# Kernel tuning notes

Measured on AMD Instinct MI355X. Metric: run time of the kernel, lower is better.

## Reference

```python
import jax, jax.numpy as jnp
import numpy as np
import math

PC_MIN_X, PC_MIN_Y = 0.0, -40.0
VOXEL = 0.05
STRIDE = 8
PE_CH = 16
NEG_SLOPE = 0.01
BN_EPS = 1e-5


def _grid_points():
    # get_pseudo_points: centers of stride-8 BEV cells
    xs = np.arange(0.2, 70.4, 0.4, dtype=np.float32)    # 176
    ys = np.arange(-39.8, 40.2, 0.4, dtype=np.float32)  # 200
    gx, gy = np.meshgrid(xs, ys)                        # (200, 176)
    return jnp.asarray(np.stack([gx, gy], -1).reshape(-1, 2))  # [P, 2]


def _pe3d(D, H, W):
    ch = PE_CH
    div = jnp.exp(jnp.arange(0, ch, 2, dtype=jnp.float32) * (-math.log(10000.0) / ch))
    def enc(n):
        t = jnp.arange(n, dtype=jnp.float32)[:, None] * div[None, :]
        return jnp.concatenate([jnp.sin(t), jnp.cos(t)], axis=-1)  # [n, ch]
    pex = jnp.broadcast_to(enc(D)[:, None, None, :], (D, H, W, ch))
    pey = jnp.broadcast_to(enc(H)[None, :, None, :], (D, H, W, ch))
    pez = jnp.broadcast_to(enc(W)[None, None, :, :], (D, H, W, ch))
    return jnp.concatenate([pex, pey, pez], axis=-1).transpose(3, 0, 1, 2)  # [3*ch, D, H, W]


def _bn_lrelu(h, g, b):
    # eval-mode BatchNorm3d with running_mean=0, running_var=1, then LeakyReLU(0.01)
    h = h * (g / np.sqrt(1.0 + BN_EPS))[None, :, None, None, None] + b[None, :, None, None, None]
    return jnp.where(h >= 0, h, NEG_SLOPE * h)


def _dvf(x, w1, b1, g1, be1, w2, b2, g2, be2, w3, b3):
    N, C, D, H, W = x.shape
    pe = _pe3d(D, H, W)  # [48, D, H, W]
    feats = jnp.concatenate([x, jnp.broadcast_to(pe[None], (N,) + pe.shape)], axis=1)
    h = jnp.einsum('ncdhw,oc->nodhw', feats, w1) + b1[None, :, None, None, None]
    h = _bn_lrelu(h, g1, be1)
    h = jnp.einsum('ncdhw,oc->nodhw', h, w2) + b2[None, :, None, None, None]
    h = _bn_lrelu(h, g2, be2)
    logits = jnp.einsum('ncdhw,oc->nodhw', h, w3) + b3[None, :, None, None, None]  # [N,1,D,H,W]
    wts = jax.nn.softmax(logits, axis=2)  # softmax over depth D
    return (x * wts).reshape(N, C * D, H, W)


def _bilinear(im, x, y):
    # im: (H, W, C), x/y: (P,)  -- faithful to bilinear_interpolate_torch
    H, W = im.shape[0], im.shape[1]
    xf = jnp.floor(x).astype(jnp.int32)
    yf = jnp.floor(y).astype(jnp.int32)
    x0 = jnp.clip(xf, 0, W - 1)
    x1 = jnp.clip(xf + 1, 0, W - 1)
    y0 = jnp.clip(yf, 0, H - 1)
    y1 = jnp.clip(yf + 1, 0, H - 1)
    Ia, Ib, Ic, Id = im[y0, x0], im[y1, x0], im[y0, x1], im[y1, x1]
    x0f, x1f = x0.astype(x.dtype), x1.astype(x.dtype)
    y0f, y1f = y0.astype(y.dtype), y1.astype(y.dtype)
    wa = (x1f - x) * (y1f - y)
    wb = (x1f - x) * (y - y0f)
    wc = (x - x0f) * (y1f - y)
    wd = (x - x0f) * (y - y0f)
    return Ia * wa[:, None] + Ib * wb[:, None] + Ic * wc[:, None] + Id * wd[:, None]


def _rot(p, theta):
    c, s = jnp.cos(theta), jnp.sin(theta)
    return jnp.stack([p[:, 0] * c - p[:, 1] * s, p[:, 0] * s + p[:, 1] * c], axis=-1)


def _bev_align_one(feat, th_prev, th_cur, grid):
    # feat: [C', H, W]; X_TRANS modeled as z-rotation: fwd(current) then inverse(previous)
    Hh, Ww = feat.shape[1], feat.shape[2]
    p = _rot(grid, th_cur)
    p = _rot(p, -th_prev)
    xi = (p[:, 0] - PC_MIN_X) / VOXEL / STRIDE
    yi = (p[:, 1] - PC_MIN_Y) / VOXEL / STRIDE
    out = _bilinear(feat.transpose(1, 2, 0), xi, yi)  # [P, C']
    return out.reshape(Hh, Ww, -1).transpose(2, 0, 1)


def setup_inputs() -> dict:
    key = jax.random.key(0)
    ks = jax.random.split(key, 16)
    N, C, D, H, W = 4, 64, 2, 200, 176
    IN1 = PE_CH * 3 + C  # 112
    inp = {
        'x0': jax.random.normal(ks[0], (N, C, D, H, W), jnp.float32),
        'x1': jax.random.normal(ks[1], (N, C, D, H, W), jnp.float32),
        'transform_param': jax.random.normal(ks[2], (N, 2), jnp.float32) * 0.3,
        'w1': jax.random.normal(ks[3], (C, IN1), jnp.float32) * 0.05,
        'b1': jax.random.normal(ks[4], (C,), jnp.float32) * 0.05,
        'g1': jax.random.uniform(ks[5], (C,), jnp.float32, 0.5, 1.5),
        'be1': jax.random.normal(ks[6], (C,), jnp.float32) * 0.05,
        'w2': jax.random.normal(ks[7], (C // 2, C), jnp.float32) * 0.05,
        'b2': jax.random.normal(ks[8], (C // 2,), jnp.float32) * 0.05,
        'g2': jax.random.uniform(ks[9], (C // 2,), jnp.float32, 0.5, 1.5),
        'be2': jax.random.normal(ks[10], (C // 2,), jnp.float32) * 0.05,
        'w3': jax.random.normal(ks[11], (1, C // 2), jnp.float32) * 0.05,
        'b3': jax.random.normal(ks[12], (1,), jnp.float32) * 0.05,
    }
    return inp


def reference(x0, x1, transform_param, w1, b1, g1, be1, w2, b2, g2, be2, w3, b3):
    mlp = (w1, b1, g1, be1, w2, b2, g2, be2, w3, b3)
    f0 = _dvf(x0, *mlp)  # rot 0: [N, C*D, H, W]
    f1 = _dvf(x1, *mlp)  # rot 1
    grid = _grid_points()
    aligned = jax.vmap(lambda f, tp: _bev_align_one(f, tp[0], tp[1], grid))(f1, transform_param)
    return jnp.maximum(f0, aligned)  # ALIGN_METHOD='max' over stacked feats
```

## Files before the change

### kernel.cpp

```cpp
#include <hip/hip_runtime.h>
#include <cmath>

#define HW   35200
#define CD   128

typedef short bf16x8 __attribute__((ext_vector_type(8)));
typedef float f32x4  __attribute__((ext_vector_type(4)));

union Frag { unsigned u[4]; bf16x8 v; };

#define OFF_W1B   0
#define OFF_W2B   3072
#define OFF_TD    4096
#define OFF_B2F   4224
#define OFF_W3F   4256
#define OFF_PE    4288
#define OFF_F0B   567488
#define OFF_F1B   9578688

__device__ __forceinline__ float lrelu(float v) { return v >= 0.f ? v : 0.01f * v; }
__device__ __forceinline__ unsigned short f2bf(float f) {
  unsigned u = __float_as_uint(f);
  u = (u + 0x7fffu + ((u >> 16) & 1u)) >> 16;
  return (unsigned short)u;
}
__device__ __forceinline__ float bflo(unsigned u) { return __uint_as_float(u << 16); }
__device__ __forceinline__ float bfhi(unsigned u) { return __uint_as_float(u & 0xffff0000u); }

__global__ void setup_kernel(const float* __restrict__ w1, const float* __restrict__ b1,
                             const float* __restrict__ g1, const float* __restrict__ be1,
                             const float* __restrict__ w2, const float* __restrict__ b2,
                             const float* __restrict__ g2, const float* __restrict__ be2,
                             const float* __restrict__ w3, const float* __restrict__ b3,
                             float* __restrict__ ws) {
  const float RS = rsqrtf(1.0f + 1e-5f);
  unsigned short* w1b = (unsigned short*)(ws + OFF_W1B);
  unsigned short* w2b = (unsigned short*)(ws + OFF_W2B);
  unsigned short* pe  = (unsigned short*)(ws + OFF_PE);
  int i = blockIdx.x * blockDim.x + threadIdx.x;
  if (i < 6144) {
    int e = i & 7, l = (i >> 3) & 63, nt = (i >> 9) & 3, kh = i >> 11;
    int n = nt * 16 + (l & 15);
    int k = kh * 32 + (l >> 4) * 8 + e;
    int col = (kh < 2) ? k : (80 + (k - 64));
    w1b[i] = f2bf(w1[n * 112 + col] * (g1[n] * RS));
    return;
  }
  i -= 6144;
  if (i < 2048) {
    int e = i & 7, l = (i >> 3) & 63, nt = (i >> 9) & 1, kh = i >> 10;
    int n = nt * 16 + (l & 15);
    int k = kh * 32 + (l >> 4) * 8 + e;
    w2b[i] = f2bf(w2[n * 64 + k] * (g2[n] * RS));
    return;
  }
  i -= 2048;
  if (i < 128) {
    int d = i >> 6, o = i & 63;
    float a = 0.f;
    for (int j = 0; j < 8; ++j) {
      float dv = expf((float)(2 * j) * (-0.5756462732485115f));
      float t  = (float)d * dv;
      a += w1[o * 112 + 64 + j] * sinf(t) + w1[o * 112 + 72 + j] * cosf(t);
    }
    ws[OFF_TD + d * 64 + o] = (g1[o] * RS) * (b1[o] + a) + be1[o];
    return;
  }
  i -= 128;
  if (i < 32) { ws[OFF_B2F + i] = b2[i] * (g2[i] * RS) + be2[i]; return; }
  i -= 32;
  if (i < 32) { ws[OFF_W3F + i] = w3[i]; return; }
  i -= 32;
  if (i < 563200) {
    int hw = i >> 4, j = i & 15;
    int h = hw / 176, w = hw - h * 176;
    int jj = j & 7;
    float dv = expf((float)(2 * jj) * (-0.5756462732485115f));
    if (j < 8) {
      float t = (float)h * dv;
      pe[hw * 32 + jj]      = f2bf(sinf(t));
      pe[hw * 32 + 8 + jj]  = f2bf(cosf(t));
    } else {
      float t = (float)w * dv;
      pe[hw * 32 + 16 + jj] = f2bf(sinf(t));
      pe[hw * 32 + 24 + jj] = f2bf(cosf(t));
    }
  }
}

__global__ __launch_bounds__(256, 4)
void mlp_kernel(const float* __restrict__ x0, const float* __restrict__ x1,
                const float* __restrict__ wtab,
                unsigned short* __restrict__ f0b, unsigned short* __restrict__ f1b) {
  __shared__ alignas(16) unsigned short Hs[8 * 128 * 8];
  __shared__ float wts[2][64];

  const int t    = threadIdx.x;
  const int lane = t & 63;
  const int wv   = __builtin_amdgcn_readfirstlane(t >> 6);
  const int g    = lane >> 4;
  const int li   = lane & 15;
  const int n    = blockIdx.y;
  const int inp  = blockIdx.z;
  const int hw0  = blockIdx.x * 64;
  const int pxs  = wv * 16 + li;
  const float* xn = (inp ? x1 : x0) + (size_t)n * CD * HW;
  unsigned short* dst = inp ? f1b : f0b;
  const unsigned short* w1bu = (const unsigned short*)(wtab + OFF_W1B);
  const unsigned short* w2bu = (const unsigned short*)(wtab + OFF_W2B);
  const unsigned short* peg  = (const unsigned short*)(wtab + OFF_PE);

  float xf[2][2][8];
#pragma unroll
  for (int ti = 0; ti < 2; ++ti)
#pragma unroll
    for (int kh = 0; kh < 2; ++kh)
#pragma unroll
      for (int e = 0; e < 8; ++e) {
        const int c = kh * 32 + g * 8 + e;
        xf[ti][kh][e] = xn[(size_t)(c * 2 + ti) * HW + hw0 + pxs];
      }
  const uint4 pev = *(const uint4*)(peg + (size_t)(hw0 + pxs) * 32 + g * 8);

  Frag xb[2][2];
#pragma unroll
  for (int ti = 0; ti < 2; ++ti)
#pragma unroll
    for (int kh = 0; kh < 2; ++kh)
#pragma unroll
      for (int q = 0; q < 4; ++q)
        xb[ti][kh].u[q] = (unsigned)f2bf(xf[ti][kh][2 * q])
                        | ((unsigned)f2bf(xf[ti][kh][2 * q + 1]) << 16);
  Frag pf;
  pf.u[0] = pev.x; pf.u[1] = pev.y; pf.u[2] = pev.z; pf.u[3] = pev.w;

  f32x4 acc[2][4];
#pragma unroll
  for (int ti = 0; ti < 2; ++ti)
#pragma unroll
    for (int nt = 0; nt < 4; ++nt) {
      const float tdv = wtab[OFF_TD + ti * 64 + nt * 16 + li];
      acc[ti][nt] = (f32x4){tdv, tdv, tdv, tdv};
    }
#pragma unroll
  for (int kh = 0; kh < 2; ++kh)
#pragma unroll
    for (int nt = 0; nt < 4; ++nt) {
      const bf16x8 b = *(const bf16x8*)&w1bu[(unsigned)((kh * 4 + nt) * 64 + lane) * 8];
      acc[0][nt] = __builtin_amdgcn_mfma_f32_16x16x32_bf16(xb[0][kh].v, b, acc[0][nt], 0, 0, 0);
      acc[1][nt] = __builtin_amdgcn_mfma_f32_16x16x32_bf16(xb[1][kh].v, b, acc[1][nt], 0, 0, 0);
    }
#pragma unroll
  for (int nt = 0; nt < 4; ++nt) {
    const bf16x8 b = *(const bf16x8*)&w1bu[(unsigned)((8 + nt) * 64 + lane) * 8];
    acc[0][nt] = __builtin_amdgcn_mfma_f32_16x16x32_bf16(pf.v, b, acc[0][nt], 0, 0, 0);
    acc[1][nt] = __builtin_amdgcn_mfma_f32_16x16x32_bf16(pf.v, b, acc[1][nt], 0, 0, 0);
  }

#pragma unroll
  for (int ti = 0; ti < 2; ++ti) {
    const int tau = wv + ti * 4;
#pragma unroll
    for (int nt = 0; nt < 4; ++nt)
#pragma unroll
      for (int r = 0; r < 4; ++r) {
        const int o   = nt * 16 + li;
        const int row = tau * 16 + g * 4 + r;
        Hs[(unsigned)((o >> 3) * 128 + row) * 8 + (o & 7)] = f2bf(lrelu(acc[ti][nt][r]));
      }
  }

  f32x4 acc2[2][2];
#pragma unroll
  for (int nt = 0; nt < 2; ++nt) {
    const float bv = wtab[OFF_B2F + nt * 16 + li];
    acc2[0][nt] = (f32x4){bv, bv, bv, bv};
    acc2[1][nt] = acc2[0][nt];
  }
#pragma unroll
  for (int kh = 0; kh < 2; ++kh) {
    const bf16x8 a0 = *(const bf16x8*)&Hs[(unsigned)((kh * 4 + g) * 128 + (wv + 0) * 16 + li) * 8];
    const bf16x8 a1 = *(const bf16x8*)&Hs[(unsigned)((kh * 4 + g) * 128 + (wv + 4) * 16 + li) * 8];
#pragma unroll
    for (int nt = 0; nt < 2; ++nt) {
      const bf16x8 b = *(const bf16x8*)&w2bu[(unsigned)((kh * 2 + nt) * 64 + lane) * 8];
      acc2[0][nt] = __builtin_amdgcn_mfma_f32_16x16x32_bf16(a0, b, acc2[0][nt], 0, 0, 0);
      acc2[1][nt] = __builtin_amdgcn_mfma_f32_16x16x32_bf16(a1, b, acc2[1][nt], 0, 0, 0);
    }
  }

  const float w3a = wtab[OFF_W3F + li];
  const float w3b = wtab[OFF_W3F + 16 + li];
  float wt0[4], wt1[4];
#pragma unroll
  for (int r = 0; r < 4; ++r) {
    float p0 = w3a * lrelu(acc2[0][0][r]) + w3b * lrelu(acc2[0][1][r]);
    float p1 = w3a * lrelu(acc2[1][0][r]) + w3b * lrelu(acc2[1][1][r]);
    p0 += __shfl_xor(p0, 1); p0 += __shfl_xor(p0, 2);
    p0 += __shfl_xor(p0, 4); p0 += __shfl_xor(p0, 8);
    p1 += __shfl_xor(p1, 1); p1 += __shfl_xor(p1, 2);
    p1 += __shfl_xor(p1, 4); p1 += __shfl_xor(p1, 8);
    wt0[r] = 1.f / (1.f + expf(p1 - p0));
    wt1[r] = 1.f / (1.f + expf(p0 - p1));
  }
  if (li == 0) {
#pragma unroll
    for (int r = 0; r < 4; ++r) {
      wts[0][wv * 16 + g * 4 + r] = wt0[r];
      wts[1][wv * 16 + g * 4 + r] = wt1[r];
    }
  }
  __syncthreads();

  const float w0  = wts[0][pxs];
  const float w1v = wts[1][pxs];
#pragma unroll
  for (int kh = 0; kh < 2; ++kh)
#pragma unroll
    for (int j = 0; j < 4; ++j) {
      const int k = kh * 16 + g * 4 + j;
      const unsigned ua = xb[0][kh].u[j];
      const unsigned ub = xb[1][kh].u[j];
      uint2 pk;
      pk.x = (unsigned)f2bf(bflo(ua) * w0) | ((unsigned)f2bf(bflo(ub) * w1v) << 16);
      pk.y = (unsigned)f2bf(bfhi(ua) * w0) | ((unsigned)f2bf(bfhi(ub) * w1v) << 16);
      *(uint2*)&dst[(((size_t)n * 32 + k) * HW + hw0 + pxs) * 4] = pk;
    }
}

__global__ __launch_bounds__(256)
void gather_max_kernel(const unsigned short* __restrict__ f0b,
                       const unsigned short* __restrict__ f1b,
                       const float* __restrict__ tp,
                       float* __restrict__ out) {
  const int orig = blockIdx.x;
  const int xcd = orig & 7, idx = orig >> 3;
  const int tile = (xcd < 6 ? xcd * 69 : 6 * 69 + (xcd - 6) * 68) + idx;

  const int tix = threadIdx.x;
  const int px  = tix & 63;
  const int q   = tix >> 6;
  const int n   = blockIdx.y;
  const int hw  = tile * 64 + px;
  const int h   = hw / 176;
  const int w   = hw - h * 176;

  const float thp = tp[n * 2 + 0], thc = tp[n * 2 + 1];
  const float gx = 0.2f + 0.4f * (float)w;
  const float gy = -39.8f + 0.4f * (float)h;
  const float c1 = cosf(thc),  s1v = sinf(thc);
  const float p1x = gx * c1 - gy * s1v;
  const float p1y = gx * s1v + gy * c1;
  const float c2 = cosf(-thp), s2v = sinf(-thp);
  const float p2x = p1x * c2 - p1y * s2v;
  const float p2y = p1x * s2v + p1y * c2;
  const float xi = p2x / 0.05f / 8.f;
  const float yi = (p2y - (-40.f)) / 0.05f / 8.f;

  const float xf = floorf(xi), yf = floorf(yi);
  const int x0i = (int)xf, y0i = (int)yf;
  const int x0c = min(max(x0i,     0), 175);
  const int x1c = min(max(x0i + 1, 0), 175);
  const int y0c = min(max(y0i,     0), 199);
  const int y1c = min(max(y0i + 1, 0), 199);
  const float x0f = (float)x0c, x1f = (float)x1c;
  const float y0f = (float)y0c, y1f = (float)y1c;
  const float wa = (x1f - xi) * (y1f - yi);
  const float wb = (x1f - xi) * (yi - y0f);
  const float wc = (xi - x0f) * (y1f - yi);
  const float wd = (xi - x0f) * (yi - y0f);
  const int ta = y0c * 176 + x0c, tb = y1c * 176 + x0c;
  const int tc = y0c * 176 + x1c, td = y1c * 176 + x1c;

#pragma unroll
  for (int i = 0; i < 8; ++i) {
    const int k = q * 8 + i;
    const int cd0 = k * 4;
    const unsigned short* fp1 = f1b + ((size_t)n * 32 + k) * HW * 4;
    const uint2 Ia = *(const uint2*)(fp1 + (size_t)ta * 4);
    const uint2 Ib = *(const uint2*)(fp1 + (size_t)tb * 4);
    const uint2 Ic = *(const uint2*)(fp1 + (size_t)tc * 4);
    const uint2 Id = *(const uint2*)(fp1 + (size_t)td * 4);
    float4 sv;
    sv.x = bflo(Ia.x) * wa + bflo(Ib.x) * wb + bflo(Ic.x) * wc + bflo(Id.x) * wd;
    sv.y = bfhi(Ia.x) * wa + bfhi(Ib.x) * wb + bfhi(Ic.x) * wc + bfhi(Id.x) * wd;
    sv.z = bflo(Ia.y) * wa + bflo(Ib.y) * wb + bflo(Ic.y) * wc + bflo(Id.y) * wd;
    sv.w = bfhi(Ia.y) * wa + bfhi(Ib.y) * wb + bfhi(Ic.y) * wc + bfhi(Id.y) * wd;

    const uint2 F0 = *(const uint2*)(f0b + (((size_t)n * 32 + k) * HW + hw) * 4);

    float* op = out + ((size_t)n * CD + cd0) * HW + hw;
    op[0]              = fmaxf(bflo(F0.x), sv.x);
    op[HW]             = fmaxf(bfhi(F0.x), sv.y);
    op[2 * (size_t)HW] = fmaxf(bflo(F0.y), sv.z);
    op[3 * (size_t)HW] = fmaxf(bfhi(F0.y), sv.w);
  }
}

extern "C" void kernel_launch(void* const* d_in, const int* in_sizes, int n_in,
                              void* d_out, int out_size, void* d_ws, size_t ws_size,
                              hipStream_t stream) {
  const float* x0  = (const float*)d_in[0];
  const float* x1  = (const float*)d_in[1];
  const float* tp  = (const float*)d_in[2];
  const float* w1  = (const float*)d_in[3];
  const float* b1  = (const float*)d_in[4];
  const float* g1  = (const float*)d_in[5];
  const float* be1 = (const float*)d_in[6];
  const float* w2  = (const float*)d_in[7];
  const float* b2  = (const float*)d_in[8];
  const float* g2  = (const float*)d_in[9];
  const float* be2 = (const float*)d_in[10];
  const float* w3  = (const float*)d_in[11];
  const float* b3  = (const float*)d_in[12];
  float* ws = (float*)d_ws;
  unsigned short* f0b = (unsigned short*)(ws + OFF_F0B);
  unsigned short* f1b = (unsigned short*)(ws + OFF_F1B);

  setup_kernel<<<2233, 256, 0, stream>>>(w1, b1, g1, be1, w2, b2, g2, be2, w3, b3, ws);

  dim3 g1d(550, 4, 2);
  mlp_kernel<<<g1d, 256, 0, stream>>>(x0, x1, ws, f0b, f1b);

  dim3 g2d(550, 4);
  gather_max_kernel<<<g2d, 256, 0, stream>>>(f0b, f1b, tp, (float*)d_out);
}
```

Before: 90.62 us.

## Replace shared-memory softmax weight exchange with shuffles and use packed bf16 conversion

```diff
diff --git a/kernel.cpp b/kernel.cpp
--- a/kernel.cpp
+++ b/kernel.cpp
@@ -1,4 +1,5 @@
 #include <hip/hip_runtime.h>
+#include <hip/hip_bf16.h>
 #include <cmath>
 
 #define HW   35200
@@ -20,9 +21,14 @@
 
 __device__ __forceinline__ float lrelu(float v) { return v >= 0.f ? v : 0.01f * v; }
 __device__ __forceinline__ unsigned short f2bf(float f) {
-  unsigned u = __float_as_uint(f);
-  u = (u + 0x7fffu + ((u >> 16) & 1u)) >> 16;
-  return (unsigned short)u;
+  union { __hip_bfloat16 h; unsigned short u; } c;
+  c.h = __float2bfloat16(f);
+  return c.u;
+}
+__device__ __forceinline__ unsigned pack2bf(float lo, float hi) {
+  union { __hip_bfloat162 h2; unsigned u; } c;
+  c.h2 = __float22bfloat162_rn(float2{lo, hi});
+  return c.u;
 }
 __device__ __forceinline__ float bflo(unsigned u) { return __uint_as_float(u << 16); }
 __device__ __forceinline__ float bfhi(unsigned u) { return __uint_as_float(u & 0xffff0000u); }
@@ -88,12 +94,11 @@
   }
 }
 
-__global__ __launch_bounds__(256, 4)
+__global__ __launch_bounds__(256)
 void mlp_kernel(const float* __restrict__ x0, const float* __restrict__ x1,
                 const float* __restrict__ wtab,
                 unsigned short* __restrict__ f0b, unsigned short* __restrict__ f1b) {
   __shared__ alignas(16) unsigned short Hs[8 * 128 * 8];
-  __shared__ float wts[2][64];
 
   const int t    = threadIdx.x;
   const int lane = t & 63;
@@ -129,8 +134,7 @@
     for (int kh = 0; kh < 2; ++kh)
 #pragma unroll
       for (int q = 0; q < 4; ++q)
-        xb[ti][kh].u[q] = (unsigned)f2bf(xf[ti][kh][2 * q])
-                        | ((unsigned)f2bf(xf[ti][kh][2 * q + 1]) << 16);
+        xb[ti][kh].u[q] = pack2bf(xf[ti][kh][2 * q], xf[ti][kh][2 * q + 1]);
   Frag pf;
   pf.u[0] = pev.x; pf.u[1] = pev.y; pf.u[2] = pev.z; pf.u[3] = pev.w;
 
@@ -203,17 +207,16 @@
     wt0[r] = 1.f / (1.f + expf(p1 - p0));
     wt1[r] = 1.f / (1.f + expf(p0 - p1));
   }
-  if (li == 0) {
-#pragma unroll
-    for (int r = 0; r < 4; ++r) {
-      wts[0][wv * 16 + g * 4 + r] = wt0[r];
-      wts[1][wv * 16 + g * 4 + r] = wt1[r];
-    }
-  }
-  __syncthreads();
-
-  const float w0  = wts[0][pxs];
-  const float w1v = wts[1][pxs];
+
+  const int src = (li >> 2) << 4;
+  const float a0 = __shfl(wt0[0], src), b0 = __shfl(wt1[0], src);
+  const float a1 = __shfl(wt0[1], src), b1v = __shfl(wt1[1], src);
+  const float a2 = __shfl(wt0[2], src), b2v = __shfl(wt1[2], src);
+  const float a3 = __shfl(wt0[3], src), b3v = __shfl(wt1[3], src);
+  const int r = li & 3;
+  const float w0  = (r == 0) ? a0 : (r == 1) ? a1 : (r == 2) ? a2 : a3;
+  const float w1v = (r == 0) ? b0 : (r == 1) ? b1v : (r == 2) ? b2v : b3v;
+
 #pragma unroll
   for (int kh = 0; kh < 2; ++kh)
 #pragma unroll
@@ -222,8 +225,8 @@
       const unsigned ua = xb[0][kh].u[j];
       const unsigned ub = xb[1][kh].u[j];
       uint2 pk;
-      pk.x = (unsigned)f2bf(bflo(ua) * w0) | ((unsigned)f2bf(bflo(ub) * w1v) << 16);
-      pk.y = (unsigned)f2bf(bfhi(ua) * w0) | ((unsigned)f2bf(bfhi(ub) * w1v) << 16);
+      pk.x = pack2bf(bflo(ua) * w0, bflo(ub) * w1v);
+      pk.y = pack2bf(bfhi(ua) * w0, bfhi(ub) * w1v);
       *(uint2*)&dst[(((size_t)n * 32 + k) * HW + hw0 + pxs) * 4] = pk;
     }
 }
```

Result: slower. 93.01 us (+2.6%).
